# Kernel optimization log

Measured on AMD Instinct MI355X. Metric: run time of the kernel, lower is better.

Reference implementation:

```python
import jax, jax.numpy as jnp
import numpy as np

STEP_SIZE = 0.3333          # module default self.step_size
N_STEPS = 4                 # >= ceil(halfWidth/step) for sigma=6, size_factor=1; extra steps are masked to 0
REF_SIZE = 1024.0           # IndexHelper.input_size_factor() reference resolution


def _bilinear(img, px, py):
    """Bilinear sample img [B,C,H,W] at normalized coords px,py [B,H,W] in [0,1].
    Pixel centers at (j+0.5)/W (grid_sample align_corners=False convention); border clamp."""
    B, C, H, W = img.shape
    fx = px * W - 0.5
    fy = py * H - 0.5
    x0 = jnp.floor(fx)
    y0 = jnp.floor(fy)
    wx = (fx - x0)[:, None]  # [B,1,H,W]
    wy = (fy - y0)[:, None]
    x0i = jnp.clip(x0.astype(jnp.int32), 0, W - 1)
    x1i = jnp.clip(x0i + 1, 0, W - 1)
    y0i = jnp.clip(y0.astype(jnp.int32), 0, H - 1)
    y1i = jnp.clip(y0i + 1, 0, H - 1)
    gather = jax.vmap(lambda im, yi, xi: im[:, yi, xi])  # per-batch advanced indexing -> [B,C,H,W]
    v00 = gather(img, y0i, x0i)
    v01 = gather(img, y0i, x1i)
    v10 = gather(img, y1i, x0i)
    v11 = gather(img, y1i, x1i)
    top = v00 * (1.0 - wx) + v01 * wx
    bot = v10 * (1.0 - wx) + v11 * wx
    return top * (1.0 - wy) + bot * wy


def _forward(x, tangent, sigma):
    B, C, H, W = x.shape
    dt = x.dtype
    size_factor = min(H, W) / REF_SIZE           # i.input_size_factor()
    sig = sigma.reshape(-1, 1, 1, 1) * size_factor  # precisionFactor = 1.0
    half_width = 2.0 * sig
    two_sigma2 = 2.0 * sig * sig
    step = 1.0 / (STEP_SIZE * size_factor)       # step = i.view(1/step_size), mode=None scaling

    # p_start: normalized pixel-center coords, channel 0 = x (width), channel 1 = y (height)
    ys, xs = jnp.meshgrid((jnp.arange(H, dtype=dt) + 0.5) / H,
                          (jnp.arange(W, dtype=dt) + 0.5) / W, indexing="ij")
    p_start = jnp.broadcast_to(jnp.stack([xs, ys])[None], (B, 2, H, W))
    tex = jnp.array([W, H], dtype=dt).reshape(1, 2, 1, 1)  # i.tex_size()

    def march(direction):
        v0 = direction
        p0 = p_start + v0 / tex

        def body(carry, it):
            c, c_sum, p, v = carry
            r = (it + 1.0) * step                       # r = step, step+step, ...
            k = jnp.exp(-r * r / two_sigma2)            # [B,1,1,1]
            k = jnp.where(r < half_width, k, 0.0)
            px, py = p[:, 0], p[:, 1]
            inb = (px >= 0.0) & (px < 1.0) & (py >= 0.0) & (py < 1.0)
            k = k * inb[:, None].astype(dt)             # [B,1,H,W]
            c = c + _bilinear(x, px, py) * k
            c_sum = c_sum + k
            tf = _bilinear(tangent, px, py)
            vt = jnp.sum(v * tf, axis=1, keepdims=True)
            tf = jnp.where(vt < 0.0, -tf, tf)           # keep marching direction consistent
            p = p + tf / tex
            return (c, c_sum, p, tf), None

        init = (jnp.zeros_like(x), jnp.zeros((B, 1, H, W), dt), p0, v0)
        (c, c_sum, _, _), _ = jax.lax.scan(body, init, jnp.arange(N_STEPS, dtype=dt))
        return c, c_sum

    c1, s1 = march(tangent)      # smoothed(C, Sum, tangent_sampled)
    c2, s2 = march(-tangent)     # smoothed(C, Sum, -tangent_sampled)
    return (x + c1 + c2) / (1.0 + s1 + s2)


def setup_inputs() -> dict:
    key = jax.random.key(0)
    k1, k2 = jax.random.split(key)
    B, C, H, W = 2, 3, 1024, 1024
    x = jax.random.normal(k1, (B, C, H, W), jnp.float32)
    # tangent: unit-length per-pixel flow direction field
    theta = jax.random.uniform(k2, (B, 1, H, W), jnp.float32, 0.0, 2.0 * np.pi)
    tangent = jnp.concatenate([jnp.cos(theta), jnp.sin(theta)], axis=1)
    sigma = jnp.full((B,), 6.0, jnp.float32)  # smoothing width in pixels
    return {"x": x, "tangent": tangent, "sigma": sigma}


def reference(x, tangent, sigma):
    return _forward(x, tangent, sigma)
```

## Files before the change

kernel.cpp:

```cpp
#include <hip/hip_runtime.h>

constexpr int Bb = 2, Cc = 3, Hh = 1024, Ww = 1024;
constexpr int HWp = Hh * Ww;
constexpr int N_STEPS = 4;
constexpr int TS = 16;
constexpr int HALO = 6;
constexpr int TD = TS + 2 * HALO;
constexpr int TSTR = TD + 1;

struct Corn { int o00, o01, o10, o11; float wx, wy, omx, omy; };

__device__ __forceinline__ Corn mkcorn_int(float px, float py, int ox, int oy) {
#pragma clang fp contract(off)
    float fx = px - 0.5f;
    float fy = py - 0.5f;
    float fx0 = floorf(fx), fy0 = floorf(fy);
    Corn c;
    c.wx = fx - fx0;  c.wy = fy - fy0;
    c.omx = 1.0f - c.wx;  c.omy = 1.0f - c.wy;
    int o = ((int)fy0 - oy) * TSTR + ((int)fx0 - ox);
    c.o00 = o;        c.o01 = o + 1;
    c.o10 = o + TSTR; c.o11 = o + TSTR + 1;
    return c;
}

__device__ __forceinline__ Corn mkcorn_bor(float px, float py, int ox, int oy) {
#pragma clang fp contract(off)
    float fx = px - 0.5f;
    float fy = py - 0.5f;
    float fx0 = floorf(fx), fy0 = floorf(fy);
    Corn c;
    c.wx = fx - fx0;  c.wy = fy - fy0;
    c.omx = 1.0f - c.wx;  c.omy = 1.0f - c.wy;
    int x0 = (int)fx0, y0 = (int)fy0;
    int x0i = min(max(x0, 0), Ww - 1);
    int x1i = min(x0i + 1, Ww - 1);
    int y0i = min(max(y0, 0), Hh - 1);
    int y1i = min(y0i + 1, Hh - 1);
    int lx0 = x0i - ox, lx1 = x1i - ox;
    int ly0 = y0i - oy, ly1 = y1i - oy;
    c.o00 = ly0 * TSTR + lx0;  c.o01 = ly0 * TSTR + lx1;
    c.o10 = ly1 * TSTR + lx0;  c.o11 = ly1 * TSTR + lx1;
    return c;
}

__device__ __forceinline__ float bsamp(const float* p, const Corn& c) {
#pragma clang fp contract(off)
    float v00 = p[c.o00], v01 = p[c.o01], v10 = p[c.o10], v11 = p[c.o11];
    float top = v00 * c.omx + v01 * c.wx;
    float bot = v10 * c.omx + v11 * c.wx;
    return top * c.omy + bot * c.wy;
}

template <bool BORDER>
__device__ __forceinline__ void run_tile(
    const float* __restrict__ x, const float* __restrict__ tg,
    const float* __restrict__ sg, float* __restrict__ out,
    float (&lds)[5][TD * TSTR])
{
#pragma clang fp contract(off)
    const int tx0 = blockIdx.x * TS, ty0 = blockIdx.y * TS;
    const int b = blockIdx.z;
    const int tid = threadIdx.x;

    const float* xp  = x  + (size_t)b * Cc * HWp;
    const float* txp = tg + (size_t)b * 2 * HWp;
    const float* planes[5] = { xp, xp + HWp, xp + 2 * HWp, txp, txp + HWp };
    const int ox = tx0 - HALO, oy = ty0 - HALO;

    float sig = sg[b];
    float half_width = 2.0f * sig;
    float two_sigma2 = (2.0f * sig) * sig;
    const float stepf = (float)(1.0 / 0.3333);
    float ks[N_STEPS];
#pragma unroll
    for (int it = 0; it < N_STEPS; ++it) {
        float r = ((float)it + 1.0f) * stepf;
        float k = expf(-(r * r) / two_sigma2);
        ks[it] = (r < half_width) ? k : 0.0f;
    }

    for (int e = tid; e < TD * TD; e += 256) {
        int r = e / TD, cc = e - r * TD;
        int gy = oy + r, gx = ox + cc;
        if (BORDER) {
            gy = min(max(gy, 0), Hh - 1);
            gx = min(max(gx, 0), Ww - 1);
        }
        int g = gy * Ww + gx;
#pragma unroll
        for (int pl = 0; pl < 5; ++pl)
            lds[pl][r * TSTR + cc] = planes[pl][g];
    }
    __syncthreads();

    const int lx = tid & (TS - 1), ly = tid >> 4;
    const int j = tx0 + lx, i = ty0 + ly;
    const int ctr = (HALO + ly) * TSTR + (HALO + lx);

    const float psx = (float)j + 0.5f;
    const float psy = (float)i + 0.5f;

    float v0x = lds[3][ctr];
    float v0y = lds[4][ctr];

    float c1a = 0.f, c1b = 0.f, c1c = 0.f, s1 = 0.f;
    float c2a = 0.f, c2b = 0.f, c2c = 0.f, s2 = 0.f;

#pragma unroll
    for (int d = 0; d < 2; ++d) {
        float vx = d ? -v0x : v0x;
        float vy = d ? -v0y : v0y;
        float px = psx + vx;
        float py = psy + vy;
        float a0 = 0.f, a1 = 0.f, a2 = 0.f, as = 0.f;
#pragma unroll
        for (int it = 0; it < N_STEPS; ++it) {
            Corn c = BORDER ? mkcorn_bor(px, py, ox, oy)
                            : mkcorn_int(px, py, ox, oy);
            if (ks[it] != 0.0f) {
                float w = ks[it];
                if (BORDER) {
                    bool inb = (px >= 0.0f) && (px < 1024.0f) &&
                               (py >= 0.0f) && (py < 1024.0f);
                    w = inb ? w : 0.0f;
                }
                a0 += bsamp(lds[0], c) * w;
                a1 += bsamp(lds[1], c) * w;
                a2 += bsamp(lds[2], c) * w;
                as += w;
            }
            if (it == N_STEPS - 1) break;
            float tfx = bsamp(lds[3], c);
            float tfy = bsamp(lds[4], c);
            float vt = (vx * tfx) + (vy * tfy);
            if (vt < 0.0f) { tfx = -tfx; tfy = -tfy; }
            px = px + tfx;
            py = py + tfy;
            vx = tfx; vy = tfy;
        }
        if (d == 0) { c1a = a0; c1b = a1; c1c = a2; s1 = as; }
        else        { c2a = a0; c2b = a1; c2c = a2; s2 = as; }
    }

    const int pix = i * Ww + j;
    float xc0 = lds[0][ctr], xc1 = lds[1][ctr], xc2 = lds[2][ctr];
    float denom = (1.0f + s1) + s2;
    float* op = out + (size_t)b * Cc * HWp;
    op[pix]           = ((xc0 + c1a) + c2a) / denom;
    op[pix + HWp]     = ((xc1 + c1b) + c2b) / denom;
    op[pix + 2 * HWp] = ((xc2 + c1c) + c2c) / denom;
}

__global__ __launch_bounds__(256) void flow_smooth_kernel(
    const float* __restrict__ x,
    const float* __restrict__ tg,
    const float* __restrict__ sg,
    float* __restrict__ out)
{
    __shared__ float lds[5][TD * TSTR];
    const bool border = (blockIdx.x == 0) || (blockIdx.x == gridDim.x - 1) ||
                        (blockIdx.y == 0) || (blockIdx.y == gridDim.y - 1);
    if (border) run_tile<true >(x, tg, sg, out, lds);
    else        run_tile<false>(x, tg, sg, out, lds);
}

extern "C" void kernel_launch(void* const* d_in, const int* in_sizes, int n_in,
                              void* d_out, int out_size, void* d_ws, size_t ws_size,
                              hipStream_t stream) {
    const float* x = nullptr; const float* tg = nullptr; const float* sg = nullptr;
    for (int t = 0; t < n_in; ++t) {
        if (in_sizes[t] == Bb * Cc * HWp)      x  = (const float*)d_in[t];
        else if (in_sizes[t] == Bb * 2 * HWp)  tg = (const float*)d_in[t];
        else                                   sg = (const float*)d_in[t];
    }
    float* out = (float*)d_out;

    dim3 block(256, 1, 1);
    dim3 grid(Ww / TS, Hh / TS, Bb);
    flow_smooth_kernel<<<grid, block, 0, stream>>>(x, tg, sg, out);
}
```

Measured before the change: 123.2 us.

## Pack color and tangent-x into float4 LDS, fuse bilinear math with FMA

Interleaves the three color channels and the tangent x-component into one float4 shared-memory array, so each bilinear corner becomes a single 128-bit LDS read instead of four scalar reads. The final march step is peeled out so it skips the unused tangent sampling, and the colour interpolation now uses fused multiply-adds. Launch bounds request 8 waves per SIMD to raise occupancy. The FMA contraction changes rounding slightly against the reference, and float4 LDS accesses at scattered offsets may hit bank conflicts.

```diff
diff --git a/kernel.cpp b/kernel.cpp
--- a/kernel.cpp
+++ b/kernel.cpp
@@ -44,19 +44,11 @@
     return c;
 }
 
-__device__ __forceinline__ float bsamp(const float* p, const Corn& c) {
-#pragma clang fp contract(off)
-    float v00 = p[c.o00], v01 = p[c.o01], v10 = p[c.o10], v11 = p[c.o11];
-    float top = v00 * c.omx + v01 * c.wx;
-    float bot = v10 * c.omx + v11 * c.wx;
-    return top * c.omy + bot * c.wy;
-}
-
 template <bool BORDER>
 __device__ __forceinline__ void run_tile(
     const float* __restrict__ x, const float* __restrict__ tg,
     const float* __restrict__ sg, float* __restrict__ out,
-    float (&lds)[5][TD * TSTR])
+    float4 (&colS)[TD * TSTR], float (&tyS)[TD * TSTR])
 {
 #pragma clang fp contract(off)
     const int tx0 = blockIdx.x * TS, ty0 = blockIdx.y * TS;
@@ -65,7 +57,7 @@
 
     const float* xp  = x  + (size_t)b * Cc * HWp;
     const float* txp = tg + (size_t)b * 2 * HWp;
-    const float* planes[5] = { xp, xp + HWp, xp + 2 * HWp, txp, txp + HWp };
+    const float* typ = txp + HWp;
     const int ox = tx0 - HALO, oy = ty0 - HALO;
 
     float sig = sg[b];
@@ -88,9 +80,10 @@
             gx = min(max(gx, 0), Ww - 1);
         }
         int g = gy * Ww + gx;
-#pragma unroll
-        for (int pl = 0; pl < 5; ++pl)
-            lds[pl][r * TSTR + cc] = planes[pl][g];
+        float4 q;
+        q.x = xp[g]; q.y = xp[g + HWp]; q.z = xp[g + 2 * HWp]; q.w = txp[g];
+        colS[r * TSTR + cc] = q;
+        tyS [r * TSTR + cc] = typ[g];
     }
     __syncthreads();
 
@@ -101,8 +94,9 @@
     const float psx = (float)j + 0.5f;
     const float psy = (float)i + 0.5f;
 
-    float v0x = lds[3][ctr];
-    float v0y = lds[4][ctr];
+    const float4 ctrq = colS[ctr];
+    const float v0x = ctrq.w;
+    const float v0y = tyS[ctr];
 
     float c1a = 0.f, c1b = 0.f, c1c = 0.f, s1 = 0.f;
     float c2a = 0.f, c2b = 0.f, c2c = 0.f, s2 = 0.f;
@@ -114,10 +108,13 @@
         float px = psx + vx;
         float py = psy + vy;
         float a0 = 0.f, a1 = 0.f, a2 = 0.f, as = 0.f;
+
 #pragma unroll
-        for (int it = 0; it < N_STEPS; ++it) {
+        for (int it = 0; it < N_STEPS - 1; ++it) {
             Corn c = BORDER ? mkcorn_bor(px, py, ox, oy)
                             : mkcorn_int(px, py, ox, oy);
+            float4 q00 = colS[c.o00], q01 = colS[c.o01];
+            float4 q10 = colS[c.o10], q11 = colS[c.o11];
             if (ks[it] != 0.0f) {
                 float w = ks[it];
                 if (BORDER) {
@@ -125,44 +122,77 @@
                                (py >= 0.0f) && (py < 1024.0f);
                     w = inb ? w : 0.0f;
                 }
-                a0 += bsamp(lds[0], c) * w;
-                a1 += bsamp(lds[1], c) * w;
-                a2 += bsamp(lds[2], c) * w;
+                float t0 = fmaf(q01.x, c.wx, q00.x * c.omx);
+                float b0 = fmaf(q11.x, c.wx, q10.x * c.omx);
+                a0 = fmaf(fmaf(b0, c.wy, t0 * c.omy), w, a0);
+                float t1 = fmaf(q01.y, c.wx, q00.y * c.omx);
+                float b1 = fmaf(q11.y, c.wx, q10.y * c.omx);
+                a1 = fmaf(fmaf(b1, c.wy, t1 * c.omy), w, a1);
+                float t2 = fmaf(q01.z, c.wx, q00.z * c.omx);
+                float b2 = fmaf(q11.z, c.wx, q10.z * c.omx);
+                a2 = fmaf(fmaf(b2, c.wy, t2 * c.omy), w, a2);
                 as += w;
             }
-            if (it == N_STEPS - 1) break;
-            float tfx = bsamp(lds[3], c);
-            float tfy = bsamp(lds[4], c);
+            float y00 = tyS[c.o00], y01 = tyS[c.o01];
+            float y10 = tyS[c.o10], y11 = tyS[c.o11];
+            float xt = q00.w * c.omx + q01.w * c.wx;
+            float xb = q10.w * c.omx + q11.w * c.wx;
+            float tfx = xt * c.omy + xb * c.wy;
+            float yt = y00 * c.omx + y01 * c.wx;
+            float yb = y10 * c.omx + y11 * c.wx;
+            float tfy = yt * c.omy + yb * c.wy;
             float vt = (vx * tfx) + (vy * tfy);
             if (vt < 0.0f) { tfx = -tfx; tfy = -tfy; }
             px = px + tfx;
             py = py + tfy;
             vx = tfx; vy = tfy;
         }
+        if (ks[N_STEPS - 1] != 0.0f) {
+            Corn c = BORDER ? mkcorn_bor(px, py, ox, oy)
+                            : mkcorn_int(px, py, ox, oy);
+            float w = ks[N_STEPS - 1];
+            if (BORDER) {
+                bool inb = (px >= 0.0f) && (px < 1024.0f) &&
+                           (py >= 0.0f) && (py < 1024.0f);
+                w = inb ? w : 0.0f;
+            }
+            float4 q00 = colS[c.o00], q01 = colS[c.o01];
+            float4 q10 = colS[c.o10], q11 = colS[c.o11];
+            float t0 = fmaf(q01.x, c.wx, q00.x * c.omx);
+            float b0 = fmaf(q11.x, c.wx, q10.x * c.omx);
+            a0 = fmaf(fmaf(b0, c.wy, t0 * c.omy), w, a0);
+            float t1 = fmaf(q01.y, c.wx, q00.y * c.omx);
+            float b1 = fmaf(q11.y, c.wx, q10.y * c.omx);
+            a1 = fmaf(fmaf(b1, c.wy, t1 * c.omy), w, a1);
+            float t2 = fmaf(q01.z, c.wx, q00.z * c.omx);
+            float b2 = fmaf(q11.z, c.wx, q10.z * c.omx);
+            a2 = fmaf(fmaf(b2, c.wy, t2 * c.omy), w, a2);
+            as += w;
+        }
         if (d == 0) { c1a = a0; c1b = a1; c1c = a2; s1 = as; }
         else        { c2a = a0; c2b = a1; c2c = a2; s2 = as; }
     }
 
     const int pix = i * Ww + j;
-    float xc0 = lds[0][ctr], xc1 = lds[1][ctr], xc2 = lds[2][ctr];
     float denom = (1.0f + s1) + s2;
     float* op = out + (size_t)b * Cc * HWp;
-    op[pix]           = ((xc0 + c1a) + c2a) / denom;
-    op[pix + HWp]     = ((xc1 + c1b) + c2b) / denom;
-    op[pix + 2 * HWp] = ((xc2 + c1c) + c2c) / denom;
-}
-
-__global__ __launch_bounds__(256) void flow_smooth_kernel(
+    op[pix]           = ((ctrq.x + c1a) + c2a) / denom;
+    op[pix + HWp]     = ((ctrq.y + c1b) + c2b) / denom;
+    op[pix + 2 * HWp] = ((ctrq.z + c1c) + c2c) / denom;
+}
+
+__global__ __launch_bounds__(256, 8) void flow_smooth_kernel(
     const float* __restrict__ x,
     const float* __restrict__ tg,
     const float* __restrict__ sg,
     float* __restrict__ out)
 {
-    __shared__ float lds[5][TD * TSTR];
+    __shared__ float4 colS[TD * TSTR];
+    __shared__ float  tyS [TD * TSTR];
     const bool border = (blockIdx.x == 0) || (blockIdx.x == gridDim.x - 1) ||
                         (blockIdx.y == 0) || (blockIdx.y == gridDim.y - 1);
-    if (border) run_tile<true >(x, tg, sg, out, lds);
-    else        run_tile<false>(x, tg, sg, out, lds);
+    if (border) run_tile<true >(x, tg, sg, out, colS, tyS);
+    else        run_tile<false>(x, tg, sg, out, colS, tyS);
 }
 
 extern "C" void kernel_launch(void* const* d_in, const int* in_sizes, int n_in,
```

Result: slower. 130.9 us (+6.2%).

## Interleave both march directions and truncate steps by wave-uniform live-kernel count

Applied to the files above, without the earlier changes.

The two opposite-direction marches are interleaved so their LDS gathers and arithmetic can overlap. A wave-uniform count of non-zero Gaussian weights (read via readfirstlane) is used to stop marching early, so dead steps skip both the colour sampling and the tangent advection. The colour bilinear is rewritten as four precomputed corner weights with fmaf, and launch bounds now request higher occupancy. The fmaf reformulation changes rounding relative to the reference's non-contracted arithmetic, and the occupancy hint may force register spills.

```diff
diff --git a/kernel.cpp b/kernel.cpp
--- a/kernel.cpp
+++ b/kernel.cpp
@@ -2,7 +2,6 @@
 
 constexpr int Bb = 2, Cc = 3, Hh = 1024, Ww = 1024;
 constexpr int HWp = Hh * Ww;
-constexpr int N_STEPS = 4;
 constexpr int TS = 16;
 constexpr int HALO = 6;
 constexpr int TD = TS + 2 * HALO;
@@ -44,14 +43,6 @@
     return c;
 }
 
-__device__ __forceinline__ float bsamp(const float* p, const Corn& c) {
-#pragma clang fp contract(off)
-    float v00 = p[c.o00], v01 = p[c.o01], v10 = p[c.o10], v11 = p[c.o11];
-    float top = v00 * c.omx + v01 * c.wx;
-    float bot = v10 * c.omx + v11 * c.wx;
-    return top * c.omy + bot * c.wy;
-}
-
 template <bool BORDER>
 __device__ __forceinline__ void run_tile(
     const float* __restrict__ x, const float* __restrict__ tg,
@@ -72,13 +63,16 @@
     float half_width = 2.0f * sig;
     float two_sigma2 = (2.0f * sig) * sig;
     const float stepf = (float)(1.0 / 0.3333);
-    float ks[N_STEPS];
+    float kv[4];
 #pragma unroll
-    for (int it = 0; it < N_STEPS; ++it) {
+    for (int it = 0; it < 4; ++it) {
         float r = ((float)it + 1.0f) * stepf;
         float k = expf(-(r * r) / two_sigma2);
-        ks[it] = (r < half_width) ? k : 0.0f;
-    }
+        kv[it] = (r < half_width) ? k : 0.0f;
+    }
+    const float k0 = kv[0], k1 = kv[1], k2 = kv[2], k3 = kv[3];
+    const int nlive = __builtin_amdgcn_readfirstlane(
+        (k0 != 0.0f) + (k1 != 0.0f) + (k2 != 0.0f) + (k3 != 0.0f));
 
     for (int e = tid; e < TD * TD; e += 256) {
         int r = e / TD, cc = e - r * TD;
@@ -101,58 +95,99 @@
     const float psx = (float)j + 0.5f;
     const float psy = (float)i + 0.5f;
 
-    float v0x = lds[3][ctr];
-    float v0y = lds[4][ctr];
-
-    float c1a = 0.f, c1b = 0.f, c1c = 0.f, s1 = 0.f;
-    float c2a = 0.f, c2b = 0.f, c2c = 0.f, s2 = 0.f;
-
-#pragma unroll
-    for (int d = 0; d < 2; ++d) {
-        float vx = d ? -v0x : v0x;
-        float vy = d ? -v0y : v0y;
-        float px = psx + vx;
-        float py = psy + vy;
-        float a0 = 0.f, a1 = 0.f, a2 = 0.f, as = 0.f;
-#pragma unroll
-        for (int it = 0; it < N_STEPS; ++it) {
-            Corn c = BORDER ? mkcorn_bor(px, py, ox, oy)
-                            : mkcorn_int(px, py, ox, oy);
-            if (ks[it] != 0.0f) {
-                float w = ks[it];
-                if (BORDER) {
-                    bool inb = (px >= 0.0f) && (px < 1024.0f) &&
-                               (py >= 0.0f) && (py < 1024.0f);
-                    w = inb ? w : 0.0f;
+    const float v0x = lds[3][ctr];
+    const float v0y = lds[4][ctr];
+
+    float pxA = psx + v0x, pyA = psy + v0y, vxA = v0x, vyA = v0y;
+    float pxB = psx - v0x, pyB = psy - v0y, vxB = -v0x, vyB = -v0y;
+    float aA0 = 0.f, aA1 = 0.f, aA2 = 0.f, asA = 0.f;
+    float aB0 = 0.f, aB1 = 0.f, aB2 = 0.f, asB = 0.f;
+
+#define MKC(C, PX, PY)                                                      \
+    Corn C = BORDER ? mkcorn_bor(PX, PY, ox, oy)                            \
+                    : mkcorn_int(PX, PY, ox, oy)
+
+#define COLORSTEP(C, PX, PY, KW, A0, A1, A2, AS) do {                       \
+    float w_ = (KW);                                                        \
+    if (BORDER) {                                                           \
+        bool inb_ = ((PX) >= 0.0f) && ((PX) < 1024.0f) &&                   \
+                    ((PY) >= 0.0f) && ((PY) < 1024.0f);                     \
+        w_ = inb_ ? w_ : 0.0f;                                              \
+    }                                                                       \
+    float w00_ = C.omx * C.omy, w01_ = C.wx * C.omy;                        \
+    float w10_ = C.omx * C.wy,  w11_ = C.wx * C.wy;                         \
+    float s0_ = fmaf(w01_, lds[0][C.o01], w00_ * lds[0][C.o00]);            \
+    s0_ = fmaf(w10_, lds[0][C.o10], s0_);                                   \
+    s0_ = fmaf(w11_, lds[0][C.o11], s0_);                                   \
+    A0 = fmaf(s0_, w_, A0);                                                 \
+    float s1_ = fmaf(w01_, lds[1][C.o01], w00_ * lds[1][C.o00]);            \
+    s1_ = fmaf(w10_, lds[1][C.o10], s1_);                                   \
+    s1_ = fmaf(w11_, lds[1][C.o11], s1_);                                   \
+    A1 = fmaf(s1_, w_, A1);                                                 \
+    float s2_ = fmaf(w01_, lds[2][C.o01], w00_ * lds[2][C.o00]);            \
+    s2_ = fmaf(w10_, lds[2][C.o10], s2_);                                   \
+    s2_ = fmaf(w11_, lds[2][C.o11], s2_);                                   \
+    A2 = fmaf(s2_, w_, A2);                                                 \
+    AS += w_;                                                               \
+} while (0)
+
+#define ADVSTEP(C, PX, PY, VX, VY) do {                                     \
+    float x00_ = lds[3][C.o00], x01_ = lds[3][C.o01];                       \
+    float x10_ = lds[3][C.o10], x11_ = lds[3][C.o11];                       \
+    float y00_ = lds[4][C.o00], y01_ = lds[4][C.o01];                       \
+    float y10_ = lds[4][C.o10], y11_ = lds[4][C.o11];                       \
+    float xt_ = x00_ * C.omx + x01_ * C.wx;                                 \
+    float xb_ = x10_ * C.omx + x11_ * C.wx;                                 \
+    float tfx_ = xt_ * C.omy + xb_ * C.wy;                                  \
+    float yt_ = y00_ * C.omx + y01_ * C.wx;                                 \
+    float yb_ = y10_ * C.omx + y11_ * C.wx;                                 \
+    float tfy_ = yt_ * C.omy + yb_ * C.wy;                                  \
+    float vt_ = ((VX) * tfx_) + ((VY) * tfy_);                              \
+    if (vt_ < 0.0f) { tfx_ = -tfx_; tfy_ = -tfy_; }                         \
+    PX = (PX) + tfx_;  PY = (PY) + tfy_;                                    \
+    VX = tfx_;  VY = tfy_;                                                  \
+} while (0)
+
+    if (nlive >= 1) {
+        MKC(cA0, pxA, pyA);  MKC(cB0, pxB, pyB);
+        COLORSTEP(cA0, pxA, pyA, k0, aA0, aA1, aA2, asA);
+        COLORSTEP(cB0, pxB, pyB, k0, aB0, aB1, aB2, asB);
+        if (nlive >= 2) {
+            ADVSTEP(cA0, pxA, pyA, vxA, vyA);
+            ADVSTEP(cB0, pxB, pyB, vxB, vyB);
+            MKC(cA1, pxA, pyA);  MKC(cB1, pxB, pyB);
+            COLORSTEP(cA1, pxA, pyA, k1, aA0, aA1, aA2, asA);
+            COLORSTEP(cB1, pxB, pyB, k1, aB0, aB1, aB2, asB);
+            if (nlive >= 3) {
+                ADVSTEP(cA1, pxA, pyA, vxA, vyA);
+                ADVSTEP(cB1, pxB, pyB, vxB, vyB);
+                MKC(cA2, pxA, pyA);  MKC(cB2, pxB, pyB);
+                COLORSTEP(cA2, pxA, pyA, k2, aA0, aA1, aA2, asA);
+                COLORSTEP(cB2, pxB, pyB, k2, aB0, aB1, aB2, asB);
+                if (nlive >= 4) {
+                    ADVSTEP(cA2, pxA, pyA, vxA, vyA);
+                    ADVSTEP(cB2, pxB, pyB, vxB, vyB);
+                    MKC(cA3, pxA, pyA);  MKC(cB3, pxB, pyB);
+                    COLORSTEP(cA3, pxA, pyA, k3, aA0, aA1, aA2, asA);
+                    COLORSTEP(cB3, pxB, pyB, k3, aB0, aB1, aB2, asB);
                 }
-                a0 += bsamp(lds[0], c) * w;
-                a1 += bsamp(lds[1], c) * w;
-                a2 += bsamp(lds[2], c) * w;
-                as += w;
             }
-            if (it == N_STEPS - 1) break;
-            float tfx = bsamp(lds[3], c);
-            float tfy = bsamp(lds[4], c);
-            float vt = (vx * tfx) + (vy * tfy);
-            if (vt < 0.0f) { tfx = -tfx; tfy = -tfy; }
-            px = px + tfx;
-            py = py + tfy;
-            vx = tfx; vy = tfy;
         }
-        if (d == 0) { c1a = a0; c1b = a1; c1c = a2; s1 = as; }
-        else        { c2a = a0; c2b = a1; c2c = a2; s2 = as; }
-    }
+    }
+#undef MKC
+#undef COLORSTEP
+#undef ADVSTEP
 
     const int pix = i * Ww + j;
     float xc0 = lds[0][ctr], xc1 = lds[1][ctr], xc2 = lds[2][ctr];
-    float denom = (1.0f + s1) + s2;
+    float denom = (1.0f + asA) + asB;
     float* op = out + (size_t)b * Cc * HWp;
-    op[pix]           = ((xc0 + c1a) + c2a) / denom;
-    op[pix + HWp]     = ((xc1 + c1b) + c2b) / denom;
-    op[pix + 2 * HWp] = ((xc2 + c1c) + c2c) / denom;
-}
-
-__global__ __launch_bounds__(256) void flow_smooth_kernel(
+    op[pix]           = ((xc0 + aA0) + aB0) / denom;
+    op[pix + HWp]     = ((xc1 + aA1) + aB1) / denom;
+    op[pix + 2 * HWp] = ((xc2 + aA2) + aB2) / denom;
+}
+
+__global__ __launch_bounds__(256, 8) void flow_smooth_kernel(
     const float* __restrict__ x,
     const float* __restrict__ tg,
     const float* __restrict__ sg,
```

Result: no change. 123.2 us (+0.1%).
